# Performance work log

Hardware: AMD Instinct MI355X
Metric: run time of the kernel (lower is better)

## Reference

```python
import itertools
import jax, jax.numpy as jnp
import numpy as np


def setup_inputs() -> dict:
    key = jax.random.key(0)
    k1, k2 = jax.random.split(key)
    B, X, Y, Z, C = 2, 160, 192, 160, 1
    vol = jax.random.normal(k1, (B, X, Y, Z, C), dtype=jnp.float32)
    trf = jax.random.normal(k2, (B, X, Y, Z, 3), dtype=jnp.float32)  # dense displacement field
    return {"vol": vol, "trf": trf}


def _warp(vol, trf):
    # vol: [B, *spatial, C]; trf: [B, *spatial, nd] displacement (indexing='ij')
    B = vol.shape[0]
    spatial = vol.shape[1:-1]
    nd = len(spatial)
    C = vol.shape[-1]
    N = int(np.prod(spatial))

    grids = jnp.meshgrid(*[jnp.arange(s, dtype=jnp.float32) for s in spatial], indexing="ij")
    # absolute sample locations per dim: [B, *spatial]
    loc = [grids[d][None] + trf[..., d] for d in range(nd)]

    max_loc = [s - 1 for s in spatial]
    loc0 = [jnp.clip(jnp.floor(loc[d]), 0.0, max_loc[d]) for d in range(nd)]
    loc1 = [jnp.clip(loc0[d] + 1.0, 0.0, max_loc[d]) for d in range(nd)]
    clipped = [jnp.clip(loc[d], 0.0, max_loc[d]) for d in range(nd)]
    # neurite weight convention: weight for corner bit 0 is (loc1 - loc), for bit 1 is (1 - that)
    w1 = [loc1[d] - clipped[d] for d in range(nd)]   # weight when corner uses loc0
    w0 = [1.0 - w1[d] for d in range(nd)]            # weight when corner uses loc1
    i0 = [loc0[d].astype(jnp.int32) for d in range(nd)]
    i1 = [loc1[d].astype(jnp.int32) for d in range(nd)]

    vol_flat = vol.reshape(B, N, C)

    out = jnp.zeros((B,) + spatial + (C,), dtype=vol.dtype)
    for corner in itertools.product([0, 1], repeat=nd):
        subs = [(i1[d] if corner[d] else i0[d]) for d in range(nd)]
        ind = subs[0]
        for d in range(1, nd):
            ind = ind * spatial[d] + subs[d]  # row-major sub2ind
        vals = jnp.take_along_axis(vol_flat, ind.reshape(B, N)[..., None], axis=1)
        vals = vals.reshape((B,) + spatial + (C,))
        wt = (w0[0] if corner[0] else w1[0])
        for d in range(1, nd):
            wt = wt * (w0[d] if corner[d] else w1[d])
        out = out + wt[..., None] * vals
    return out


def reference(vol, trf):
    # indexing='ij', single_transform=False, fill_value=None (clamp to edge), linear interp.
    # The layer also passes trf through unchanged; we return the warped volume.
    return _warp(vol, trf)
```

## Files before the change

kernel.cpp:

```cpp
#include <hip/hip_runtime.h>

constexpr int B = 2, X = 160, Y = 192, Z = 160;
constexpr int TXs = 8, TYs = 8, TZs = 16;
constexpr int XT = X / TXs, YT = Y / TYs, ZT = Z / TZs;
constexpr int NTILES = B * XT * YT * ZT;
constexpr int NXCD = 8;
constexpr int CHUNK = NTILES / NXCD;
constexpr int RX = 16, RY = 16, RZ = 24;
constexpr int NROWS = RX * RY;
constexpr int RSTRIDE = RZ + 1;
constexpr int LDSF = NROWS * RSTRIDE;

typedef float f32x4 __attribute__((ext_vector_type(4)));
typedef float f32x2a __attribute__((ext_vector_type(2), aligned(4)));

__global__ __launch_bounds__(256, 6) void warp_kernel(
    const float* __restrict__ vol,
    const float* __restrict__ trf,
    float* __restrict__ out)
{
    __shared__ float lds[LDSF];

    const int tid = threadIdx.x;
    const int bid = blockIdx.x;

    const int eff = (bid & (NXCD - 1)) * CHUNK + (bid >> 3);

    int tz = eff % ZT;
    int r  = eff / ZT;
    int ty = r % YT;
    int r2 = r / YT;
    int tx = r2 % XT;
    int b  = r2 / XT;

    const int xs = tx * TXs - 4;
    const int ys = ty * TYs - 4;
    const int zs = tz * TZs - 4;

    {
        int row = (tid * 171) >> 10;
        int j   = tid - 6 * row;
#pragma unroll
        for (int k = 0; k < 6; ++k) {
            int xi = row >> 4;
            int yi = row & 15;
            int xg = min(max(xs + xi, 0), X - 1);
            int yg = min(max(ys + yi, 0), Y - 1);
            int zg = min(max(zs + 4 * j, 0), Z - 4);
            const f32x4 v = *reinterpret_cast<const f32x4*>(
                vol + ((size_t)(b * X + xg) * Y + yg) * Z + zg);
            int a = row * RSTRIDE + 4 * j;
            lds[a + 0] = v.x;
            lds[a + 1] = v.y;
            lds[a + 2] = v.z;
            lds[a + 3] = v.w;
            int jn = j + 4;
            bool wrap = (jn >= 6);
            j   = wrap ? jn - 6 : jn;
            row += wrap ? 43 : 42;
        }
    }
    __syncthreads();

    int zq = tid & 3;
    int ly = (tid >> 2) & 7;
    int lx = tid >> 5;
    int x  = tx * TXs + lx;
    int y  = ty * TYs + ly;
    int z0v = tz * TZs + 4 * zq;

    size_t vid0 = ((size_t)(b * X + x) * Y + y) * Z + z0v;

    const f32x4* tp = reinterpret_cast<const f32x4*>(trf + vid0 * 3);
    f32x4 t0 = tp[0], t1 = tp[1], t2 = tp[2];
    float d[12] = {t0.x, t0.y, t0.z, t0.w,
                   t1.x, t1.y, t1.z, t1.w,
                   t2.x, t2.y, t2.z, t2.w};

    const float mx = (float)(X - 1), my = (float)(Y - 1), mz = (float)(Z - 1);
    const float fx = (float)x, fy = (float)y;
    const int bX = b * X;

    float res[4];
#pragma unroll
    for (int e = 0; e < 4; ++e) {
        float lxf = fx + d[3 * e + 0];
        float lyf = fy + d[3 * e + 1];
        float lzf = (float)(z0v + e) + d[3 * e + 2];

        float lx0 = fminf(fmaxf(floorf(lxf), 0.0f), mx);
        float lx1 = fminf(lx0 + 1.0f, mx);
        float clx = fminf(fmaxf(lxf, 0.0f), mx);
        float wxA = lx1 - clx, wxB = 1.0f - wxA;
        int ix0 = (int)lx0, ix1 = (int)lx1;

        float ly0 = fminf(fmaxf(floorf(lyf), 0.0f), my);
        float ly1 = fminf(ly0 + 1.0f, my);
        float cly = fminf(fmaxf(lyf, 0.0f), my);
        float wyA = ly1 - cly, wyB = 1.0f - wyA;
        int iy0 = (int)ly0, iy1 = (int)ly1;

        float lz0 = fminf(fmaxf(floorf(lzf), 0.0f), mz);
        float lz1 = fminf(lz0 + 1.0f, mz);
        float clz = fminf(fmaxf(lzf, 0.0f), mz);
        float wzA = lz1 - clz, wzB = 1.0f - wzA;
        int iz0 = (int)lz0, iz1 = (int)lz1;

        bool edge = (iz1 == iz0);
        float wzAe = edge ? 1.0f : wzA;
        float wzBe = edge ? 0.0f : wzB;

        int ux0 = ix0 - xs, ux1 = ix1 - xs;
        int uy0 = iy0 - ys, uy1 = iy1 - ys;
        int uz0 = iz0 - zs;

        bool ok = ((unsigned)ux0 < (unsigned)RX) & ((unsigned)ux1 < (unsigned)RX) &
                  ((unsigned)uy0 < (unsigned)RY) & ((unsigned)uy1 < (unsigned)RY) &
                  ((unsigned)uz0 < (unsigned)(RZ - 1));

        float v000, v001, v010, v011, v100, v101, v110, v111;
        if (ok) {
            int dY  = (iy1 > iy0) ? RSTRIDE : 0;
            int dXx = (ix1 > ix0) ? (RSTRIDE * 16) : 0;
            int r00 = ((ux0 << 4) + uy0) * RSTRIDE + uz0;
            int r01 = r00 + dY;
            int r10 = r00 + dXx;
            int r11 = r10 + dY;
            f32x2a p00 = *reinterpret_cast<const f32x2a*>(&lds[r00]);
            f32x2a p01 = *reinterpret_cast<const f32x2a*>(&lds[r01]);
            f32x2a p10 = *reinterpret_cast<const f32x2a*>(&lds[r10]);
            f32x2a p11 = *reinterpret_cast<const f32x2a*>(&lds[r11]);
            v000 = p00.x; v001 = p00.y;
            v010 = p01.x; v011 = p01.y;
            v100 = p10.x; v101 = p10.y;
            v110 = p11.x; v111 = p11.y;
        } else {
            size_t g00 = ((size_t)(bX + ix0) * Y + iy0) * Z;
            size_t g01 = ((size_t)(bX + ix0) * Y + iy1) * Z;
            size_t g10 = ((size_t)(bX + ix1) * Y + iy0) * Z;
            size_t g11 = ((size_t)(bX + ix1) * Y + iy1) * Z;
            v000 = vol[g00 + iz0];
            v001 = vol[g00 + iz1];
            v010 = vol[g01 + iz0];
            v011 = vol[g01 + iz1];
            v100 = vol[g10 + iz0];
            v101 = vol[g10 + iz1];
            v110 = vol[g11 + iz0];
            v111 = vol[g11 + iz1];
        }

        res[e] = wxA * (wyA * (wzAe * v000 + wzBe * v001) +
                        wyB * (wzAe * v010 + wzBe * v011)) +
                 wxB * (wyA * (wzAe * v100 + wzBe * v101) +
                        wyB * (wzAe * v110 + wzBe * v111));
    }

    f32x4 o;
    o.x = res[0]; o.y = res[1]; o.z = res[2]; o.w = res[3];
    *reinterpret_cast<f32x4*>(out + vid0) = o;
}

extern "C" void kernel_launch(void* const* d_in, const int* in_sizes, int n_in,
                              void* d_out, int out_size, void* d_ws, size_t ws_size,
                              hipStream_t stream) {
    const float* vol = (const float*)d_in[0];
    const float* trf = (const float*)d_in[1];
    float* out = (float*)d_out;

    warp_kernel<<<NTILES, 256, 0, stream>>>(vol, trf, out);
}
```

Measured before the change: 40.40 us.

## Store LDS halo tile as z-planes and use lerp-form trilinear weights

The shared-memory halo tile is re-laid out from z-contiguous rows with stride 25 into z-major planes of 257 floats. The eight corner samples become scalar LDS reads at fixed offsets, replacing four unaligned float2 reads, with the aim of changing the bank-access pattern. Interpolation is rewritten as clamp, floor, fraction and nested lerps, which removes the second-corner index and edge-weight computations. The in-tile check is tightened, so more edge samples take the global-memory fallback path.

```diff
diff --git a/kernel.cpp b/kernel.cpp
--- a/kernel.cpp
+++ b/kernel.cpp
@@ -7,12 +7,10 @@
 constexpr int NXCD = 8;
 constexpr int CHUNK = NTILES / NXCD;
 constexpr int RX = 16, RY = 16, RZ = 24;
-constexpr int NROWS = RX * RY;
-constexpr int RSTRIDE = RZ + 1;
-constexpr int LDSF = NROWS * RSTRIDE;
+constexpr int PLANE = RX * RY + 1;
+constexpr int LDSF = RZ * PLANE;
 
 typedef float f32x4 __attribute__((ext_vector_type(4)));
-typedef float f32x2a __attribute__((ext_vector_type(2), aligned(4)));
 
 __global__ __launch_bounds__(256, 6) void warp_kernel(
     const float* __restrict__ vol,
@@ -36,6 +34,7 @@
     const int xs = tx * TXs - 4;
     const int ys = ty * TYs - 4;
     const int zs = tz * TZs - 4;
+    const int bX = b * X;
 
     {
         int row = (tid * 171) >> 10;
@@ -48,12 +47,12 @@
             int yg = min(max(ys + yi, 0), Y - 1);
             int zg = min(max(zs + 4 * j, 0), Z - 4);
             const f32x4 v = *reinterpret_cast<const f32x4*>(
-                vol + ((size_t)(b * X + xg) * Y + yg) * Z + zg);
-            int a = row * RSTRIDE + 4 * j;
-            lds[a + 0] = v.x;
-            lds[a + 1] = v.y;
-            lds[a + 2] = v.z;
-            lds[a + 3] = v.w;
+                vol + ((size_t)(bX + xg) * Y + yg) * Z + zg);
+            int w0 = 1028 * j + row;
+            lds[w0]             = v.x;
+            lds[w0 + PLANE]     = v.y;
+            lds[w0 + 2 * PLANE] = v.z;
+            lds[w0 + 3 * PLANE] = v.w;
             int jn = j + 4;
             bool wrap = (jn >= 6);
             j   = wrap ? jn - 6 : jn;
@@ -69,7 +68,7 @@
     int y  = ty * TYs + ly;
     int z0v = tz * TZs + 4 * zq;
 
-    size_t vid0 = ((size_t)(b * X + x) * Y + y) * Z + z0v;
+    size_t vid0 = ((size_t)(bX + x) * Y + y) * Z + z0v;
 
     const f32x4* tp = reinterpret_cast<const f32x4*>(trf + vid0 * 3);
     f32x4 t0 = tp[0], t1 = tp[1], t2 = tp[2];
@@ -78,63 +77,51 @@
                    t2.x, t2.y, t2.z, t2.w};
 
     const float mx = (float)(X - 1), my = (float)(Y - 1), mz = (float)(Z - 1);
-    const float fx = (float)x, fy = (float)y;
-    const int bX = b * X;
+    const float fxc = (float)x, fyc = (float)y;
 
     float res[4];
 #pragma unroll
     for (int e = 0; e < 4; ++e) {
-        float lxf = fx + d[3 * e + 0];
-        float lyf = fy + d[3 * e + 1];
+        float lxf = fxc + d[3 * e + 0];
+        float lyf = fyc + d[3 * e + 1];
         float lzf = (float)(z0v + e) + d[3 * e + 2];
 
-        float lx0 = fminf(fmaxf(floorf(lxf), 0.0f), mx);
-        float lx1 = fminf(lx0 + 1.0f, mx);
         float clx = fminf(fmaxf(lxf, 0.0f), mx);
-        float wxA = lx1 - clx, wxB = 1.0f - wxA;
-        int ix0 = (int)lx0, ix1 = (int)lx1;
+        float flx = floorf(clx);
+        float fx  = clx - flx;
+        int   ix0 = (int)flx;
 
-        float ly0 = fminf(fmaxf(floorf(lyf), 0.0f), my);
-        float ly1 = fminf(ly0 + 1.0f, my);
         float cly = fminf(fmaxf(lyf, 0.0f), my);
-        float wyA = ly1 - cly, wyB = 1.0f - wyA;
-        int iy0 = (int)ly0, iy1 = (int)ly1;
+        float fly = floorf(cly);
+        float fy  = cly - fly;
+        int   iy0 = (int)fly;
 
-        float lz0 = fminf(fmaxf(floorf(lzf), 0.0f), mz);
-        float lz1 = fminf(lz0 + 1.0f, mz);
         float clz = fminf(fmaxf(lzf, 0.0f), mz);
-        float wzA = lz1 - clz, wzB = 1.0f - wzA;
-        int iz0 = (int)lz0, iz1 = (int)lz1;
+        float flz = floorf(clz);
+        float fz  = clz - flz;
+        int   iz0 = (int)flz;
 
-        bool edge = (iz1 == iz0);
-        float wzAe = edge ? 1.0f : wzA;
-        float wzBe = edge ? 0.0f : wzB;
+        int ux0 = ix0 - xs, uy0 = iy0 - ys, uz0 = iz0 - zs;
 
-        int ux0 = ix0 - xs, ux1 = ix1 - xs;
-        int uy0 = iy0 - ys, uy1 = iy1 - ys;
-        int uz0 = iz0 - zs;
-
-        bool ok = ((unsigned)ux0 < (unsigned)RX) & ((unsigned)ux1 < (unsigned)RX) &
-                  ((unsigned)uy0 < (unsigned)RY) & ((unsigned)uy1 < (unsigned)RY) &
+        bool ok = ((unsigned)ux0 < (unsigned)(RX - 1)) &
+                  ((unsigned)uy0 < (unsigned)(RY - 1)) &
                   ((unsigned)uz0 < (unsigned)(RZ - 1));
 
         float v000, v001, v010, v011, v100, v101, v110, v111;
         if (ok) {
-            int dY  = (iy1 > iy0) ? RSTRIDE : 0;
-            int dXx = (ix1 > ix0) ? (RSTRIDE * 16) : 0;
-            int r00 = ((ux0 << 4) + uy0) * RSTRIDE + uz0;
-            int r01 = r00 + dY;
-            int r10 = r00 + dXx;
-            int r11 = r10 + dY;
-            f32x2a p00 = *reinterpret_cast<const f32x2a*>(&lds[r00]);
-            f32x2a p01 = *reinterpret_cast<const f32x2a*>(&lds[r01]);
-            f32x2a p10 = *reinterpret_cast<const f32x2a*>(&lds[r10]);
-            f32x2a p11 = *reinterpret_cast<const f32x2a*>(&lds[r11]);
-            v000 = p00.x; v001 = p00.y;
-            v010 = p01.x; v011 = p01.y;
-            v100 = p10.x; v101 = p10.y;
-            v110 = p11.x; v111 = p11.y;
+            int w = uz0 * PLANE + (ux0 << 4) + uy0;
+            v000 = lds[w];
+            v001 = lds[w + PLANE];
+            v010 = lds[w + 1];
+            v011 = lds[w + PLANE + 1];
+            v100 = lds[w + 16];
+            v101 = lds[w + PLANE + 16];
+            v110 = lds[w + 17];
+            v111 = lds[w + PLANE + 17];
         } else {
+            int ix1 = min(ix0 + 1, X - 1);
+            int iy1 = min(iy0 + 1, Y - 1);
+            int iz1 = min(iz0 + 1, Z - 1);
             size_t g00 = ((size_t)(bX + ix0) * Y + iy0) * Z;
             size_t g01 = ((size_t)(bX + ix0) * Y + iy1) * Z;
             size_t g10 = ((size_t)(bX + ix1) * Y + iy0) * Z;
@@ -149,10 +136,13 @@
             v111 = vol[g11 + iz1];
         }
 
-        res[e] = wxA * (wyA * (wzAe * v000 + wzBe * v001) +
-                        wyB * (wzAe * v010 + wzBe * v011)) +
-                 wxB * (wyA * (wzAe * v100 + wzBe * v101) +
-                        wyB * (wzAe * v110 + wzBe * v111));
+        float c00 = v000 + fz * (v001 - v000);
+        float c01 = v010 + fz * (v011 - v010);
+        float c10 = v100 + fz * (v101 - v100);
+        float c11 = v110 + fz * (v111 - v110);
+        float c0  = c00 + fy * (c01 - c00);
+        float c1  = c10 + fy * (c11 - c10);
+        res[e] = c0 + fx * (c1 - c0);
     }
 
     f32x4 o;
```

Measured after the change: 44.71 us. 1.11x slower.
